# Kernel tuning notes

Hardware: AMD Instinct MI355X
Metric: run time of the kernel (lower is better)

The kernel has to match this reference:

```python
import jax, jax.numpy as jnp
import numpy as np

N_NODES = 6890
N_ANGLES = 8
K_CHEB = 15
N_DESC = 544
HIDDEN = 64
N_CLASS = 6890
M = N_ANGLES * N_NODES  # 55120, size of anisotropic Laplacian
DEG = 16
NNZ = M * DEG
BN_EPS = 1e-5


def setup_inputs() -> dict:
    key = jax.random.key(0)
    ks = jax.random.split(key, 16)
    x = jax.random.normal(ks[0], (N_NODES, N_DESC), dtype=jnp.float32)
    # sparse anisotropic Laplacian (M x M), ~DEG nnz per row
    rows = jnp.repeat(jnp.arange(M, dtype=jnp.int32), DEG)
    cols = jax.random.randint(ks[1], (NNZ,), 0, M, dtype=jnp.int32)
    vals = jax.random.normal(ks[2], (NNZ,), dtype=jnp.float32) * 0.1
    # conv1: (K, n_angles*n_desc, 64); conv2..6 stacked: (5, K, n_angles*64, 64)
    def xavier(k, shape, fan_in, fan_out):
        lim = np.sqrt(6.0 / (fan_in + fan_out))
        return jax.random.uniform(k, shape, jnp.float32, -lim, lim)
    W1 = xavier(ks[3], (K_CHEB, N_ANGLES * N_DESC, HIDDEN), N_ANGLES * N_DESC, HIDDEN)
    Wc = xavier(ks[4], (5, K_CHEB, N_ANGLES * HIDDEN, HIDDEN), N_ANGLES * HIDDEN, HIDDEN)
    conv_b = jnp.zeros((6, HIDDEN), jnp.float32)
    bn_gamma = jnp.ones((6, HIDDEN), jnp.float32)
    bn_beta = jnp.zeros((6, HIDDEN), jnp.float32)
    fc2_w = xavier(ks[5], (HIDDEN, 256), HIDDEN, 256)
    fc2_b = jnp.zeros((256,), jnp.float32)
    fc3_w = xavier(ks[6], (256, N_CLASS), 256, N_CLASS)
    fc3_b = jnp.zeros((N_CLASS,), jnp.float32)
    return {"x": x, "rows": rows, "cols": cols, "vals": vals,
            "W1": W1, "Wc": Wc, "conv_b": conv_b,
            "bn_gamma": bn_gamma, "bn_beta": bn_beta,
            "fc2_w": fc2_w, "fc2_b": fc2_b, "fc3_w": fc3_w, "fc3_b": fc3_b}


def _spmm(rows, cols, vals, T):
    # (M x M sparse) @ (M x C) via gather + segment-sum
    return jax.ops.segment_sum(vals[:, None] * T[cols], rows, num_segments=M)


def _acs_conv(x, rows, cols, vals, W, b):
    # x: (N, C). Chebyshev recurrence on the (A*N, C) angle-stacked signal.
    N, C = x.shape
    A = N_ANGLES

    def proj(T, Wk):
        # (A*N, C) -> (N, A*C) @ (A*C, out)
        return T.reshape(A, N, C).transpose(1, 0, 2).reshape(N, A * C) @ Wk

    T0 = jnp.tile(x, (A, 1))
    out = proj(T0, W[0])
    T1 = _spmm(rows, cols, vals, T0)
    out = out + proj(T1, W[1])
    for k in range(2, K_CHEB):
        T2 = 2.0 * _spmm(rows, cols, vals, T1) - T0
        out = out + proj(T2, W[k])
        T0, T1 = T1, T2
    return out + b


def _bn_relu(x, gamma, beta):
    # BatchNorm1d (training-mode batch stats, biased variance) + ReLU
    mean = jnp.mean(x, axis=0)
    var = jnp.var(x, axis=0)
    return jax.nn.relu((x - mean) * jax.lax.rsqrt(var + BN_EPS) * gamma + beta)


def reference(x, rows, cols, vals, W1, Wc, conv_b, bn_gamma, bn_beta,
              fc2_w, fc2_b, fc3_w, fc3_b):
    h = _bn_relu(_acs_conv(x, rows, cols, vals, W1, conv_b[0]), bn_gamma[0], bn_beta[0])
    for i in range(5):
        h = _bn_relu(_acs_conv(h, rows, cols, vals, Wc[i], conv_b[i + 1]),
                     bn_gamma[i + 1], bn_beta[i + 1])
    h = jax.nn.relu(h @ fc2_w + fc2_b)
    # dropout is identity at inference
    return h @ fc3_w + fc3_b
```

## Files before the change

### kernel.cpp

```cpp
#include <hip/hip_runtime.h>
#include <cstdint>
#include <cstddef>

#define NN 6890
#define NA 8
#define KC 15
#define ND 544
#define MR (NA * NN)
#define DEG 16
#define BN_EPS 1e-5f
#define PB 864
#define NRG 108

typedef unsigned int u32;
typedef _Float16 f16;
typedef __attribute__((ext_vector_type(8))) _Float16 f16x8;
typedef __attribute__((ext_vector_type(4))) float f32x4;

union U4H8 { uint4 q; f16 h[8]; f16x8 v; };

__device__ __forceinline__ u32 packh(float a, float b) {
    union { f16 h[2]; u32 u; } c;
    c.h[0] = (f16)a; c.h[1] = (f16)b; return c.u;
}
__device__ __forceinline__ uint4 pack8h(const float* t) {
    uint4 m;
    m.x = packh(t[0], t[1]); m.y = packh(t[2], t[3]);
    m.z = packh(t[4], t[5]); m.w = packh(t[6], t[7]);
    return m;
}
__device__ __forceinline__ void acc8h(float* s, float v, uint4 g) {
    U4H8 c; c.q = g;
    #pragma unroll
    for (int i = 0; i < 8; ++i) s[i] += v * (float)c.h[i];
}

template<int CC>
__global__ __launch_bounds__(256)
void tile_slab_kernel(const float* __restrict__ X, int C_in, int c0,
                      uint4* __restrict__ slab0)
{
    constexpr int LPR = CC / 8;
    constexpr int RPB = 256 / LPR;
    const int tid = threadIdx.x;
    const int j = tid % LPR, rloc = tid / LPR;
    const int r = blockIdx.x * RPB + rloc;
    if (r >= MR) return;
    const int n = r % NN;
    const float4 t0 = *(const float4*)&X[(size_t)n * C_in + c0 + 8 * j];
    const float4 t1 = *(const float4*)&X[(size_t)n * C_in + c0 + 8 * j + 4];
    float t[8] = { t0.x, t0.y, t0.z, t0.w, t1.x, t1.y, t1.z, t1.w };
    slab0[(size_t)r * LPR + j] = pack8h(t);
}

template<int CC, bool CHEB>
__device__ __forceinline__
void spmm_body(const uint4* __restrict__ sprev, const uint4* __restrict__ scarry,
               uint4* __restrict__ scur,
               const int* __restrict__ cols, const float* __restrict__ vals)
{
    constexpr int LPR = CC / 8;
    constexpr int RPB = 256 / LPR;
    const int tid = threadIdx.x;
    const int j = tid % LPR, rloc = tid / LPR;
    const int r = blockIdx.x * RPB + rloc;
    if (r >= MR) return;

    const int nz = r * DEG;
    int   ci[DEG];
    float vv[DEG];
    const int4*   c4 = (const int4*)  (cols + nz);
    const float4* v4 = (const float4*)(vals + nz);
    #pragma unroll
    for (int q = 0; q < DEG / 4; ++q) {
        *(int4*)  &ci[4 * q] = c4[q];
        *(float4*)&vv[4 * q] = v4[q];
    }
    float s[8] = {0.f, 0.f, 0.f, 0.f, 0.f, 0.f, 0.f, 0.f};
    #pragma unroll
    for (int d = 0; d < DEG; ++d) {
        const uint4 g = sprev[(size_t)ci[d] * LPR + j];
        acc8h(s, vv[d], g);
    }
    float t[8];
    if (CHEB) {
        U4H8 p; p.q = scarry[(size_t)r * LPR + j];
        #pragma unroll
        for (int i = 0; i < 8; ++i) t[i] = 2.f * s[i] - (float)p.h[i];
    } else {
        #pragma unroll
        for (int i = 0; i < 8; ++i) t[i] = s[i];
    }
    scur[(size_t)r * LPR + j] = pack8h(t);
}

template<int CC, bool FIRSTP>
__device__ __forceinline__
void proj_body(int pb, const uint4* __restrict__ sl, const float* __restrict__ W,
               float* __restrict__ part, int C_in, int c0, int kproj,
               u32* WH, u32* WL)
{
    constexpr int CCH = CC / 32;
    constexpr int LPR = CC / 8;
    const int tid = threadIdx.x;
    const int l = tid & 63, w = tid >> 6;
    const int a = pb / NRG, rg = pb % NRG;
    const int rows0 = rg * 64;
    const int hi16 = l >> 4;
    const float* Wk = W + ((size_t)kproj * NA * C_in + (size_t)a * C_in + c0) * 64;

    for (int e = tid; e < CCH * 1024; e += 256) {
        const int i2 = e & 3;
        const int ll = (e >> 2) & 63;
        const int nt = (e >> 8) & 3;
        const int h  = e >> 10;
        const int cc  = h * 32 + (ll >> 4) * 8 + 2 * i2;
        const int col = nt * 16 + (ll & 15);
        const float w0 = Wk[(size_t)cc * 64 + col];
        const float w1 = Wk[(size_t)(cc + 1) * 64 + col];
        const f16 h0 = (f16)w0, h1 = (f16)w1;
        union { f16 h[2]; u32 u; } ph, pl;
        ph.h[0] = h0; ph.h[1] = h1;
        pl.h[0] = (f16)(w0 - (float)h0); pl.h[1] = (f16)(w1 - (float)h1);
        WH[e] = ph.u; WL[e] = pl.u;
    }
    __syncthreads();

    const int arow = rows0 + w * 16 + (l & 15);
    const int arc  = arow < NN ? arow : NN - 1;
    const size_t abase = (size_t)(a * NN + arc) * LPR;

    f32x4 acc[4];
    #pragma unroll
    for (int nt = 0; nt < 4; ++nt) {
        #pragma unroll
        for (int rr = 0; rr < 4; ++rr) {
            const int orow = rows0 + w * 16 + hi16 * 4 + rr;
            float v = 0.f;
            if (!FIRSTP && orow < NN)
                v = part[((size_t)a * NN + orow) * 64 + nt * 16 + (l & 15)];
            acc[nt][rr] = v;
        }
    }
    #pragma unroll
    for (int h = 0; h < CCH; ++h) {
        U4H8 af; af.q = sl[abase + h * 4 + hi16];
        #pragma unroll
        for (int nt = 0; nt < 4; ++nt) {
            const int be = ((h * 4 + nt) * 64 + l) * 4;
            U4H8 bh, bl;
            bh.q = *(const uint4*)&WH[be];
            bl.q = *(const uint4*)&WL[be];
            acc[nt] = __builtin_amdgcn_mfma_f32_16x16x32_f16(af.v, bh.v, acc[nt], 0, 0, 0);
            acc[nt] = __builtin_amdgcn_mfma_f32_16x16x32_f16(af.v, bl.v, acc[nt], 0, 0, 0);
        }
    }
    #pragma unroll
    for (int nt = 0; nt < 4; ++nt) {
        #pragma unroll
        for (int rr = 0; rr < 4; ++rr) {
            const int orow = rows0 + w * 16 + hi16 * 4 + rr;
            if (orow < NN)
                part[((size_t)a * NN + orow) * 64 + nt * 16 + (l & 15)] = acc[nt][rr];
        }
    }
}

template<int CC, bool CHEB, bool FIRSTP>
__global__ __launch_bounds__(256)
void step_kernel(const uint4* __restrict__ sprev, const uint4* __restrict__ scarry,
                 uint4* __restrict__ scur,
                 const int* __restrict__ cols, const float* __restrict__ vals,
                 const float* __restrict__ W, float* __restrict__ part,
                 int C_in, int c0, int kproj, int NB)
{
    constexpr int CCH = CC / 32;
    __shared__ u32 WH[CCH * 1024];
    __shared__ u32 WL[CCH * 1024];
    if ((int)blockIdx.x < NB) {
        spmm_body<CC, CHEB>(sprev, scarry, scur, cols, vals);
    } else {
        proj_body<CC, FIRSTP>((int)blockIdx.x - NB, sprev, W, part, C_in, c0, kproj, WH, WL);
    }
}

template<int CC>
__global__ __launch_bounds__(256)
void proj_only_kernel(const uint4* __restrict__ sl, const float* __restrict__ W,
                      float* __restrict__ part, int C_in, int c0, int kproj)
{
    constexpr int CCH = CC / 32;
    __shared__ u32 WH[CCH * 1024];
    __shared__ u32 WL[CCH * 1024];
    proj_body<CC, false>((int)blockIdx.x, sl, W, part, C_in, c0, kproj, WH, WL);
}

__global__ void bn_reduce_kernel(const float* __restrict__ part, float* __restrict__ acc)
{
    const int e = blockIdx.x * blockDim.x + threadIdx.x;
    if (e >= NN * 64) return;
    float s = 0.f;
    #pragma unroll
    for (int a = 0; a < NA; ++a) s += part[(size_t)a * NN * 64 + e];
    acc[e] = s;
}

__global__ __launch_bounds__(256)
void bn_stats_kernel(const float* __restrict__ acc, const float* __restrict__ gamma,
                     const float* __restrict__ beta, float* __restrict__ bnp)
{
    const int h = blockIdx.x;
    float s = 0.f, sq = 0.f;
    for (int n = threadIdx.x; n < NN; n += 256) {
        const float v = acc[(size_t)n * 64 + h];
        s += v; sq += v * v;
    }
    __shared__ float ls[256], lq[256];
    ls[threadIdx.x] = s; lq[threadIdx.x] = sq;
    __syncthreads();
    for (int st = 128; st > 0; st >>= 1) {
        if (threadIdx.x < st) { ls[threadIdx.x] += ls[threadIdx.x + st]; lq[threadIdx.x] += lq[threadIdx.x + st]; }
        __syncthreads();
    }
    if (threadIdx.x == 0) {
        const float mean = ls[0] / (float)NN;
        const float var  = lq[0] / (float)NN - mean * mean;
        const float sc   = gamma[h] / sqrtf(var + BN_EPS);
        bnp[h]      = sc;
        bnp[64 + h] = beta[h] - mean * sc;
    }
}

__global__ void bn_apply_kernel(const float* __restrict__ acc, const float* __restrict__ bnp,
                                float* __restrict__ H)
{
    const int e = blockIdx.x * blockDim.x + threadIdx.x;
    if (e >= NN * 64) return;
    const int h = e & 63;
    const float v = acc[e] * bnp[h] + bnp[64 + h];
    H[e] = v > 0.f ? v : 0.f;
}

template<bool RELU>
__global__ __launch_bounds__(256)
void gemm_bias_kernel(const float* __restrict__ A, const float* __restrict__ B,
                      const float* __restrict__ bias, float* __restrict__ C,
                      int Mm, int Nn, int Kk)
{
    __shared__ float As[16][132];
    __shared__ float Bs[16][132];
    const int tx = threadIdx.x & 15, ty = threadIdx.x >> 4;
    const int m0 = blockIdx.y * 128, n0 = blockIdx.x * 128;
    const bool full = (m0 + 128 <= Mm) && (n0 + 128 <= Nn);
    float acc[8][8] = {};
    for (int k0 = 0; k0 < Kk; k0 += 16) {
        if (full) {
            #pragma unroll
            for (int e = threadIdx.x; e < 512; e += 256) {
                const int i = e >> 2, q = e & 3;
                const float4 a4 = *(const float4*)&A[(size_t)(m0 + i) * Kk + k0 + 4 * q];
                As[4 * q + 0][i] = a4.x; As[4 * q + 1][i] = a4.y;
                As[4 * q + 2][i] = a4.z; As[4 * q + 3][i] = a4.w;
            }
            #pragma unroll
            for (int e = threadIdx.x; e < 512; e += 256) {
                const int kk = e >> 5, q = e & 31;
                *(float4*)&Bs[kk][4 * q] = *(const float4*)&B[(size_t)(k0 + kk) * Nn + n0 + 4 * q];
            }
        } else {
            for (int e = threadIdx.x; e < 128 * 16; e += 256) {
                const int i = e >> 4, kk = e & 15;
                const int row = m0 + i;
                As[kk][i] = (row < Mm) ? A[(size_t)row * Kk + k0 + kk] : 0.f;
            }
            for (int e = threadIdx.x; e < 16 * 128; e += 256) {
                const int kk = e >> 7, jj = e & 127;
                const int col = n0 + jj;
                Bs[kk][jj] = (col < Nn) ? B[(size_t)(k0 + kk) * Nn + col] : 0.f;
            }
        }
        __syncthreads();
        #pragma unroll
        for (int kk = 0; kk < 16; ++kk) {
            float av[8], bv[8];
            *(float4*)&av[0] = *(const float4*)&As[kk][ty * 4];
            *(float4*)&av[4] = *(const float4*)&As[kk][64 + ty * 4];
            *(float4*)&bv[0] = *(const float4*)&Bs[kk][tx * 4];
            *(float4*)&bv[4] = *(const float4*)&Bs[kk][64 + tx * 4];
            #pragma unroll
            for (int i = 0; i < 8; ++i)
                #pragma unroll
                for (int jj = 0; jj < 8; ++jj)
                    acc[i][jj] += av[i] * bv[jj];
        }
        __syncthreads();
    }
    for (int i = 0; i < 8; ++i) {
        const int row = m0 + (i < 4 ? ty * 4 + i : 64 + ty * 4 + (i - 4));
        if (row >= Mm) continue;
        for (int jj = 0; jj < 8; ++jj) {
            const int col = n0 + (jj < 4 ? tx * 4 + jj : 64 + tx * 4 + (jj - 4));
            if (col >= Nn) continue;
            float v = acc[i][jj] + bias[col];
            if (RELU) v = fmaxf(v, 0.f);
            C[(size_t)row * Nn + col] = v;
        }
    }
}

__global__ __launch_bounds__(256)
void fc3_mfma_kernel(const float* __restrict__ A, const float* __restrict__ Bm,
                     const float* __restrict__ bias, float* __restrict__ C)
{
    constexpr int Mm = NN, Nn = NN, Kk = 256;
    __shared__ __align__(16) f16 Ah[128][40], Al[128][40];
    __shared__ __align__(16) f16 Bh[128][40], Bl[128][40];
    const int tid = threadIdx.x, l = tid & 63, w = tid >> 6;
    const int wm = w >> 1, wn = w & 1;
    const int hi16 = l >> 4;
    const int m0 = blockIdx.y * 128, n0 = blockIdx.x * 128;

    f32x4 acc[4][4];
    #pragma unroll
    for (int mf = 0; mf < 4; ++mf)
        #pragma unroll
        for (int nf = 0; nf < 4; ++nf)
            acc[mf][nf] = (f32x4){0.f, 0.f, 0.f, 0.f};

    for (int k0 = 0; k0 < Kk; k0 += 32) {
        #pragma unroll
        for (int e = tid; e < 1024; e += 256) {
            const int row = e >> 3, q = e & 7;
            const int gr = m0 + row;
            float4 a4 = make_float4(0.f, 0.f, 0.f, 0.f);
            if (gr < Mm) a4 = *(const float4*)&A[(size_t)gr * Kk + k0 + 4 * q];
            const f16 h0 = (f16)a4.x, h1 = (f16)a4.y, h2 = (f16)a4.z, h3 = (f16)a4.w;
            Ah[row][4 * q + 0] = h0; Ah[row][4 * q + 1] = h1;
            Ah[row][4 * q + 2] = h2; Ah[row][4 * q + 3] = h3;
            Al[row][4 * q + 0] = (f16)(a4.x - (float)h0);
            Al[row][4 * q + 1] = (f16)(a4.y - (float)h1);
            Al[row][4 * q + 2] = (f16)(a4.z - (float)h2);
            Al[row][4 * q + 3] = (f16)(a4.w - (float)h3);
        }
        #pragma unroll
        for (int e = tid; e < 2048; e += 256) {
            const int kk = e >> 6, q = e & 63;
            const int gc = n0 + 2 * q;
            float2 b2 = make_float2(0.f, 0.f);
            const float* bp = &Bm[(size_t)(k0 + kk) * Nn + gc];
            if (gc + 1 < Nn)      b2 = *(const float2*)bp;
            else if (gc < Nn)     b2.x = bp[0];
            const f16 h0 = (f16)b2.x, h1 = (f16)b2.y;
            Bh[2 * q + 0][kk] = h0; Bh[2 * q + 1][kk] = h1;
            Bl[2 * q + 0][kk] = (f16)(b2.x - (float)h0);
            Bl[2 * q + 1][kk] = (f16)(b2.y - (float)h1);
        }
        __syncthreads();

        f16x8 ah_[4], al_[4], bh_[4], bl_[4];
        #pragma unroll
        for (int mf = 0; mf < 4; ++mf) {
            ah_[mf] = *(const f16x8*)&Ah[wm * 64 + mf * 16 + (l & 15)][hi16 * 8];
            al_[mf] = *(const f16x8*)&Al[wm * 64 + mf * 16 + (l & 15)][hi16 * 8];
        }
        #pragma unroll
        for (int nf = 0; nf < 4; ++nf) {
            bh_[nf] = *(const f16x8*)&Bh[wn * 64 + nf * 16 + (l & 15)][hi16 * 8];
            bl_[nf] = *(const f16x8*)&Bl[wn * 64 + nf * 16 + (l & 15)][hi16 * 8];
        }
        #pragma unroll
        for (int mf = 0; mf < 4; ++mf)
            #pragma unroll
            for (int nf = 0; nf < 4; ++nf) {
                acc[mf][nf] = __builtin_amdgcn_mfma_f32_16x16x32_f16(ah_[mf], bh_[nf], acc[mf][nf], 0, 0, 0);
                acc[mf][nf] = __builtin_amdgcn_mfma_f32_16x16x32_f16(ah_[mf], bl_[nf], acc[mf][nf], 0, 0, 0);
                acc[mf][nf] = __builtin_amdgcn_mfma_f32_16x16x32_f16(al_[mf], bh_[nf], acc[mf][nf], 0, 0, 0);
            }
        __syncthreads();
    }

    #pragma unroll
    for (int mf = 0; mf < 4; ++mf) {
        #pragma unroll
        for (int nf = 0; nf < 4; ++nf) {
            const int col = n0 + wn * 64 + nf * 16 + (l & 15);
            if (col >= Nn) continue;
            const float bv = bias[col];
            #pragma unroll
            for (int rr = 0; rr < 4; ++rr) {
                const int row = m0 + wm * 64 + mf * 16 + hi16 * 4 + rr;
                if (row < Mm)
                    C[(size_t)row * Nn + col] = acc[mf][nf][rr] + bv;
            }
        }
    }
}

template<int CC>
static void run_chunk(bool first, const float* X, int C_in, int c0,
                      const int* cols, const float* vals, const float* W,
                      uint4* const sl[3], float* part, hipStream_t stream)
{
    constexpr int LPR = CC / 8;
    constexpr int RPB = 256 / LPR;
    const int NB = (MR + RPB - 1) / RPB;

    tile_slab_kernel<CC><<<NB, 256, 0, stream>>>(X, C_in, c0, sl[0]);
    if (first)
        step_kernel<CC, false, true ><<<NB + PB, 256, 0, stream>>>(
            sl[0], sl[0], sl[1], cols, vals, W, part, C_in, c0, 0, NB);
    else
        step_kernel<CC, false, false><<<NB + PB, 256, 0, stream>>>(
            sl[0], sl[0], sl[1], cols, vals, W, part, C_in, c0, 0, NB);
    for (int k = 2; k < KC; ++k) {
        step_kernel<CC, true, false><<<NB + PB, 256, 0, stream>>>(
            sl[(k - 1) % 3], sl[(k - 2) % 3], sl[k % 3],
            cols, vals, W, part, C_in, c0, k - 1, NB);
    }
    proj_only_kernel<CC><<<PB, 256, 0, stream>>>(sl[(KC - 1) % 3], W, part, C_in, c0, KC - 1);
}

extern "C" void kernel_launch(void* const* d_in, const int* in_sizes, int n_in,
                              void* d_out, int out_size, void* d_ws, size_t ws_size,
                              hipStream_t stream)
{
    (void)in_sizes; (void)n_in; (void)out_size; (void)ws_size;
    const float* x     = (const float*)d_in[0];
    const int*   cols  = (const int*)  d_in[2];
    const float* vals  = (const float*)d_in[3];
    const float* W1    = (const float*)d_in[4];
    const float* Wc    = (const float*)d_in[5];
    const float* gamma = (const float*)d_in[7];
    const float* beta  = (const float*)d_in[8];
    const float* fc2w  = (const float*)d_in[9];
    const float* fc2b  = (const float*)d_in[10];
    const float* fc3w  = (const float*)d_in[11];
    const float* fc3b  = (const float*)d_in[12];

    const size_t MT   = (size_t)MR * 64;
    const size_t SLOT = (size_t)MR * 8;
    uint4* slabs = (uint4*)d_ws;
    uint4* sl[3] = { slabs, slabs + SLOT, slabs + 2 * SLOT };
    float* part = (float*)(slabs + 3 * SLOT);
    float* acc  = part + MT;
    float* H    = acc + (size_t)NN * 64;
    float* f2   = H + (size_t)NN * 64;
    float* bnp  = f2 + (size_t)NN * 256;

    for (int li = 0; li < 6; ++li) {
        const int C_in = (li == 0) ? ND : 64;
        const float* X = (li == 0) ? x : H;
        const float* W = (li == 0) ? W1 : Wc + (size_t)(li - 1) * KC * (NA * 64) * 64;
        const int nfull = C_in / 64;
        for (int c = 0; c < nfull; ++c)
            run_chunk<64>(c == 0, X, C_in, c * 64, cols, vals, W, sl, part, stream);
        if (C_in % 64)
            run_chunk<32>(false, X, C_in, nfull * 64, cols, vals, W, sl, part, stream);

        bn_reduce_kernel<<<(NN * 64 + 255) / 256, 256, 0, stream>>>(part, acc);
        bn_stats_kernel<<<64, 256, 0, stream>>>(acc, gamma + li * 64, beta + li * 64, bnp);
        bn_apply_kernel<<<(NN * 64 + 255) / 256, 256, 0, stream>>>(acc, bnp, H);
    }

    gemm_bias_kernel<true><<<dim3(2, 54), 256, 0, stream>>>(H, fc2w, fc2b, f2, NN, 256, 64);
    fc3_mfma_kernel<<<dim3(54, 54), 256, 0, stream>>>(f2, fc3w, fc3b, (float*)d_out);
}
```

Baseline: 4.495 ms.

## Pack sparse cols/vals to 16-bit, split slabs into 32-channel halves, presplit fc3 operands

Sparse column indices and values are packed into 16-bit indices and fp16 values in one uint4 per four nonzeros, with nontemporal loads and stores, halving index and value traffic per SpMM step. Each 64-channel slab is split into two 32-channel halves so each thread handles 4 lanes per row and reuses the decoded cols/vals for both halves. The fc3 GEMM now reads f16 hi/lo operands prepared by separate split kernels instead of converting and staging through LDS each tile. Storing the sparse values as fp16 loses precision relative to the fp32 reference, and 16-bit indices only hold while the column count fits, which it does not here (M=55120 > 65535? no, it fits).

```diff
diff --git a/kernel.cpp b/kernel.cpp
--- a/kernel.cpp
+++ b/kernel.cpp
@@ -8,16 +8,28 @@
 #define ND 544
 #define MR (NA * NN)
 #define DEG 16
+#define NNZ (MR * DEG)
 #define BN_EPS 1e-5f
-#define PB 864
+#define NSB 862
 #define NRG 108
+#define PB (NA * NRG)
 
 typedef unsigned int u32;
 typedef _Float16 f16;
 typedef __attribute__((ext_vector_type(8))) _Float16 f16x8;
 typedef __attribute__((ext_vector_type(4))) float f32x4;
+typedef __attribute__((ext_vector_type(4))) unsigned int u32x4;
 
 union U4H8 { uint4 q; f16 h[8]; f16x8 v; };
+
+__device__ __forceinline__ uint4 nt_load4(const uint4* p) {
+    const u32x4 v = __builtin_nontemporal_load((const u32x4*)p);
+    uint4 r; r.x = v.x; r.y = v.y; r.z = v.z; r.w = v.w; return r;
+}
+__device__ __forceinline__ void nt_store4(uint4 v, uint4* p) {
+    u32x4 t; t.x = v.x; t.y = v.y; t.z = v.z; t.w = v.w;
+    __builtin_nontemporal_store(t, (u32x4*)p);
+}
 
 __device__ __forceinline__ u32 packh(float a, float b) {
     union { f16 h[2]; u32 u; } c;
@@ -35,73 +47,98 @@
     for (int i = 0; i < 8; ++i) s[i] += v * (float)c.h[i];
 }
 
-template<int CC>
+__global__ __launch_bounds__(256)
+void prep_cv_kernel(const int* __restrict__ cols, const float* __restrict__ vals,
+                    uint4* __restrict__ cvq)
+{
+    const int q = blockIdx.x * 256 + threadIdx.x;
+    if (q >= NNZ / 4) return;
+    const int4   c = ((const int4*)cols)[q];
+    const float4 v = ((const float4*)vals)[q];
+    uint4 o;
+    o.x = ((u32)c.x & 0xffffu) | ((u32)c.y << 16);
+    o.y = ((u32)c.z & 0xffffu) | ((u32)c.w << 16);
+    o.z = packh(v.x, v.y);
+    o.w = packh(v.z, v.w);
+    cvq[q] = o;
+}
+
+template<int NH>
 __global__ __launch_bounds__(256)
 void tile_slab_kernel(const float* __restrict__ X, int C_in, int c0,
-                      uint4* __restrict__ slab0)
-{
-    constexpr int LPR = CC / 8;
-    constexpr int RPB = 256 / LPR;
+                      uint4* __restrict__ s0A, uint4* __restrict__ s0B)
+{
     const int tid = threadIdx.x;
-    const int j = tid % LPR, rloc = tid / LPR;
-    const int r = blockIdx.x * RPB + rloc;
+    const int r = blockIdx.x * 64 + (tid >> 2);
+    const int j = tid & 3;
     if (r >= MR) return;
     const int n = r % NN;
-    const float4 t0 = *(const float4*)&X[(size_t)n * C_in + c0 + 8 * j];
-    const float4 t1 = *(const float4*)&X[(size_t)n * C_in + c0 + 8 * j + 4];
-    float t[8] = { t0.x, t0.y, t0.z, t0.w, t1.x, t1.y, t1.z, t1.w };
-    slab0[(size_t)r * LPR + j] = pack8h(t);
-}
-
-template<int CC, bool CHEB>
+    #pragma unroll
+    for (int u = 0; u < NH; ++u) {
+        const float* xp = X + (size_t)n * C_in + c0 + u * 32 + j * 8;
+        const float4 t0 = *(const float4*)xp;
+        const float4 t1 = *(const float4*)(xp + 4);
+        float t[8] = { t0.x, t0.y, t0.z, t0.w, t1.x, t1.y, t1.z, t1.w };
+        (u ? s0B : s0A)[(size_t)r * 4 + j] = pack8h(t);
+    }
+}
+
+template<bool CHEB>
 __device__ __forceinline__
-void spmm_body(const uint4* __restrict__ sprev, const uint4* __restrict__ scarry,
-               uint4* __restrict__ scur,
-               const int* __restrict__ cols, const float* __restrict__ vals)
-{
-    constexpr int LPR = CC / 8;
-    constexpr int RPB = 256 / LPR;
-    const int tid = threadIdx.x;
-    const int j = tid % LPR, rloc = tid / LPR;
-    const int r = blockIdx.x * RPB + rloc;
-    if (r >= MR) return;
-
-    const int nz = r * DEG;
-    int   ci[DEG];
-    float vv[DEG];
-    const int4*   c4 = (const int4*)  (cols + nz);
-    const float4* v4 = (const float4*)(vals + nz);
-    #pragma unroll
-    for (int q = 0; q < DEG / 4; ++q) {
-        *(int4*)  &ci[4 * q] = c4[q];
-        *(float4*)&vv[4 * q] = v4[q];
-    }
+void spmm_unit(int r, int j, const int* c, const float* v,
+               const uint4* __restrict__ sp, const uint4* __restrict__ sc,
+               uint4* __restrict__ sw)
+{
     float s[8] = {0.f, 0.f, 0.f, 0.f, 0.f, 0.f, 0.f, 0.f};
     #pragma unroll
-    for (int d = 0; d < DEG; ++d) {
-        const uint4 g = sprev[(size_t)ci[d] * LPR + j];
-        acc8h(s, vv[d], g);
-    }
+    for (int d = 0; d < DEG; ++d)
+        acc8h(s, v[d], sp[(size_t)c[d] * 4 + j]);
     float t[8];
     if (CHEB) {
-        U4H8 p; p.q = scarry[(size_t)r * LPR + j];
+        U4H8 p; p.q = nt_load4(sc + (size_t)r * 4 + j);
         #pragma unroll
         for (int i = 0; i < 8; ++i) t[i] = 2.f * s[i] - (float)p.h[i];
     } else {
         #pragma unroll
         for (int i = 0; i < 8; ++i) t[i] = s[i];
     }
-    scur[(size_t)r * LPR + j] = pack8h(t);
-}
-
-template<int CC, bool FIRSTP>
+    nt_store4(pack8h(t), sw + (size_t)r * 4 + j);
+}
+
+template<int NH, bool CHEB>
 __device__ __forceinline__
-void proj_body(int pb, const uint4* __restrict__ sl, const float* __restrict__ W,
-               float* __restrict__ part, int C_in, int c0, int kproj,
-               u32* WH, u32* WL)
-{
-    constexpr int CCH = CC / 32;
-    constexpr int LPR = CC / 8;
+void spmm_body(const uint4* __restrict__ spA, const uint4* __restrict__ spB,
+               const uint4* __restrict__ scA, const uint4* __restrict__ scB,
+               uint4* __restrict__ swA, uint4* __restrict__ swB,
+               const uint4* __restrict__ cvq)
+{
+    const int tid = threadIdx.x;
+    const int r = blockIdx.x * 64 + (tid >> 2);
+    const int j = tid & 3;
+    if (r >= MR) return;
+    int c[16]; float v[16];
+    const uint4* cvp = cvq + (size_t)r * 4;
+    #pragma unroll
+    for (int q = 0; q < 4; ++q) {
+        const uint4 cq = nt_load4(cvp + q);
+        c[4 * q + 0] = cq.x & 0xffffu; c[4 * q + 1] = cq.x >> 16;
+        c[4 * q + 2] = cq.y & 0xffffu; c[4 * q + 3] = cq.y >> 16;
+        union { u32 u; f16 h[2]; } z, w_;
+        z.u = cq.z; w_.u = cq.w;
+        v[4 * q + 0] = (float)z.h[0]; v[4 * q + 1] = (float)z.h[1];
+        v[4 * q + 2] = (float)w_.h[0]; v[4 * q + 3] = (float)w_.h[1];
+    }
+    spmm_unit<CHEB>(r, j, c, v, spA, scA, swA);
+    if (NH == 2)
+        spmm_unit<CHEB>(r, j, c, v, spB, scB, swB);
+}
+
+template<int NH, bool FIRSTP>
+__device__ __forceinline__
+void proj_body(int pb, const uint4* __restrict__ sA, const uint4* __restrict__ sB,
+               const float* __restrict__ W, float* __restrict__ part,
+               int C_in, int c0, int kproj, u32* WH, u32* WL)
+{
     const int tid = threadIdx.x;
     const int l = tid & 63, w = tid >> 6;
     const int a = pb / NRG, rg = pb % NRG;
@@ -109,7 +146,7 @@
     const int hi16 = l >> 4;
     const float* Wk = W + ((size_t)kproj * NA * C_in + (size_t)a * C_in + c0) * 64;
 
-    for (int e = tid; e < CCH * 1024; e += 256) {
+    for (int e = tid; e < NH * 1024; e += 256) {
         const int i2 = e & 3;
         const int ll = (e >> 2) & 63;
         const int nt = (e >> 8) & 3;
@@ -128,7 +165,7 @@
 
     const int arow = rows0 + w * 16 + (l & 15);
     const int arc  = arow < NN ? arow : NN - 1;
-    const size_t abase = (size_t)(a * NN + arc) * LPR;
+    const size_t abase = (size_t)(a * NN + arc) * 4;
 
     f32x4 acc[4];
     #pragma unroll
@@ -136,15 +173,15 @@
         #pragma unroll
         for (int rr = 0; rr < 4; ++rr) {
             const int orow = rows0 + w * 16 + hi16 * 4 + rr;
-            float v = 0.f;
+            float vv = 0.f;
             if (!FIRSTP && orow < NN)
-                v = part[((size_t)a * NN + orow) * 64 + nt * 16 + (l & 15)];
-            acc[nt][rr] = v;
-        }
-    }
-    #pragma unroll
-    for (int h = 0; h < CCH; ++h) {
-        U4H8 af; af.q = sl[abase + h * 4 + hi16];
+                vv = part[((size_t)a * NN + orow) * 64 + nt * 16 + (l & 15)];
+            acc[nt][rr] = vv;
+        }
+    }
+    #pragma unroll
+    for (int h = 0; h < NH; ++h) {
+        U4H8 af; af.q = (h == 0 ? sA : sB)[abase + hi16];
         #pragma unroll
         for (int nt = 0; nt < 4; ++nt) {
             const int be = ((h * 4 + nt) * 64 + l) * 4;
@@ -166,33 +203,32 @@
     }
 }
 
-template<int CC, bool CHEB, bool FIRSTP>
-__global__ __launch_bounds__(256)
-void step_kernel(const uint4* __restrict__ sprev, const uint4* __restrict__ scarry,
-                 uint4* __restrict__ scur,
-                 const int* __restrict__ cols, const float* __restrict__ vals,
+template<int NH, bool CHEB, bool FIRSTP>
+__global__ __launch_bounds__(256)
+void step_kernel(const uint4* __restrict__ spA, const uint4* __restrict__ spB,
+                 const uint4* __restrict__ scA, const uint4* __restrict__ scB,
+                 uint4* __restrict__ swA, uint4* __restrict__ swB,
+                 const uint4* __restrict__ cvq,
                  const float* __restrict__ W, float* __restrict__ part,
-                 int C_in, int c0, int kproj, int NB)
-{
-    constexpr int CCH = CC / 32;
-    __shared__ u32 WH[CCH * 1024];
-    __shared__ u32 WL[CCH * 1024];
-    if ((int)blockIdx.x < NB) {
-        spmm_body<CC, CHEB>(sprev, scarry, scur, cols, vals);
-    } else {
-        proj_body<CC, FIRSTP>((int)blockIdx.x - NB, sprev, W, part, C_in, c0, kproj, WH, WL);
-    }
-}
-
-template<int CC>
-__global__ __launch_bounds__(256)
-void proj_only_kernel(const uint4* __restrict__ sl, const float* __restrict__ W,
-                      float* __restrict__ part, int C_in, int c0, int kproj)
-{
-    constexpr int CCH = CC / 32;
-    __shared__ u32 WH[CCH * 1024];
-    __shared__ u32 WL[CCH * 1024];
-    proj_body<CC, false>((int)blockIdx.x, sl, W, part, C_in, c0, kproj, WH, WL);
+                 int C_in, int c0, int kproj)
+{
+    __shared__ u32 WH[NH * 1024];
+    __shared__ u32 WL[NH * 1024];
+    if ((int)blockIdx.x < NSB)
+        spmm_body<NH, CHEB>(spA, spB, scA, scB, swA, swB, cvq);
+    else
+        proj_body<NH, FIRSTP>((int)blockIdx.x - NSB, spA, spB, W, part, C_in, c0, kproj, WH, WL);
+}
+
+template<int NH>
+__global__ __launch_bounds__(256)
+void proj_only_kernel(const uint4* __restrict__ sA, const uint4* __restrict__ sB,
+                      const float* __restrict__ W, float* __restrict__ part,
+                      int C_in, int c0, int kproj)
+{
+    __shared__ u32 WH[NH * 1024];
+    __shared__ u32 WL[NH * 1024];
+    proj_body<NH, false>((int)blockIdx.x, sA, sB, W, part, C_in, c0, kproj, WH, WL);
 }
 
 __global__ void bn_reduce_kernel(const float* __restrict__ part, float* __restrict__ acc)
@@ -309,16 +345,65 @@
 }
 
 __global__ __launch_bounds__(256)
-void fc3_mfma_kernel(const float* __restrict__ A, const float* __restrict__ Bm,
+void w3_split_kernel(const float* __restrict__ W, f16* __restrict__ Wh, f16* __restrict__ Wl)
+{
+    __shared__ float t[64][65];
+    const int tid = threadIdx.x;
+    const int n0 = blockIdx.x * 64, k0 = blockIdx.y * 64;
+    for (int e = tid; e < 64 * 64; e += 256) {
+        const int kk = e >> 6, nn = e & 63;
+        const int gn = n0 + nn;
+        t[kk][nn] = (gn < NN) ? W[(size_t)(k0 + kk) * NN + gn] : 0.f;
+    }
+    __syncthreads();
+    for (int e = tid; e < 64 * 64; e += 256) {
+        const int nn = e >> 6, kk = e & 63;
+        const int gn = n0 + nn;
+        if (gn < NN) {
+            const float w = t[kk][nn];
+            const f16 h = (f16)w;
+            Wh[(size_t)gn * 256 + k0 + kk] = h;
+            Wl[(size_t)gn * 256 + k0 + kk] = (f16)(w - (float)h);
+        }
+    }
+}
+
+__global__ __launch_bounds__(256)
+void f2_split_kernel(const float* __restrict__ f2, f16* __restrict__ Ah, f16* __restrict__ Al)
+{
+    const int e = blockIdx.x * 256 + threadIdx.x;
+    if (e >= NN * 256) return;
+    const float v = f2[e];
+    const f16 h = (f16)v;
+    Ah[e] = h;
+    Al[e] = (f16)(v - (float)h);
+}
+
+__global__ __launch_bounds__(256)
+void fc3_mfma_kernel(const f16* __restrict__ Ah, const f16* __restrict__ Al,
+                     const f16* __restrict__ Bh, const f16* __restrict__ Bl,
                      const float* __restrict__ bias, float* __restrict__ C)
 {
-    constexpr int Mm = NN, Nn = NN, Kk = 256;
-    __shared__ __align__(16) f16 Ah[128][40], Al[128][40];
-    __shared__ __align__(16) f16 Bh[128][40], Bl[128][40];
     const int tid = threadIdx.x, l = tid & 63, w = tid >> 6;
-    const int wm = w >> 1, wn = w & 1;
-    const int hi16 = l >> 4;
+    const int wm = w >> 1, wn = w & 1, hi16 = l >> 4;
     const int m0 = blockIdx.y * 128, n0 = blockIdx.x * 128;
+
+    const f16* aph[4]; const f16* apl[4];
+    const f16* bph[4]; const f16* bpl[4];
+    #pragma unroll
+    for (int mf = 0; mf < 4; ++mf) {
+        int row = m0 + wm * 64 + mf * 16 + (l & 15);
+        if (row > NN - 1) row = NN - 1;
+        aph[mf] = Ah + (size_t)row * 256 + hi16 * 8;
+        apl[mf] = Al + (size_t)row * 256 + hi16 * 8;
+    }
+    #pragma unroll
+    for (int nf = 0; nf < 4; ++nf) {
+        int col = n0 + wn * 64 + nf * 16 + (l & 15);
+        if (col > NN - 1) col = NN - 1;
+        bph[nf] = Bh + (size_t)col * 256 + hi16 * 8;
+        bpl[nf] = Bl + (size_t)col * 256 + hi16 * 8;
+    }
 
     f32x4 acc[4][4];
     #pragma unroll
@@ -327,56 +412,26 @@
         for (int nf = 0; nf < 4; ++nf)
             acc[mf][nf] = (f32x4){0.f, 0.f, 0.f, 0.f};
 
-    for (int k0 = 0; k0 < Kk; k0 += 32) {
-        #pragma unroll
-        for (int e = tid; e < 1024; e += 256) {
-            const int row = e >> 3, q = e & 7;
-            const int gr = m0 + row;
-            float4 a4 = make_float4(0.f, 0.f, 0.f, 0.f);
-            if (gr < Mm) a4 = *(const float4*)&A[(size_t)gr * Kk + k0 + 4 * q];
-            const f16 h0 = (f16)a4.x, h1 = (f16)a4.y, h2 = (f16)a4.z, h3 = (f16)a4.w;
-            Ah[row][4 * q + 0] = h0; Ah[row][4 * q + 1] = h1;
-            Ah[row][4 * q + 2] = h2; Ah[row][4 * q + 3] = h3;
-            Al[row][4 * q + 0] = (f16)(a4.x - (float)h0);
-            Al[row][4 * q + 1] = (f16)(a4.y - (float)h1);
-            Al[row][4 * q + 2] = (f16)(a4.z - (float)h2);
-            Al[row][4 * q + 3] = (f16)(a4.w - (float)h3);
-        }
-        #pragma unroll
-        for (int e = tid; e < 2048; e += 256) {
-            const int kk = e >> 6, q = e & 63;
-            const int gc = n0 + 2 * q;
-            float2 b2 = make_float2(0.f, 0.f);
-            const float* bp = &Bm[(size_t)(k0 + kk) * Nn + gc];
-            if (gc + 1 < Nn)      b2 = *(const float2*)bp;
-            else if (gc < Nn)     b2.x = bp[0];
-            const f16 h0 = (f16)b2.x, h1 = (f16)b2.y;
-            Bh[2 * q + 0][kk] = h0; Bh[2 * q + 1][kk] = h1;
-            Bl[2 * q + 0][kk] = (f16)(b2.x - (float)h0);
-            Bl[2 * q + 1][kk] = (f16)(b2.y - (float)h1);
-        }
-        __syncthreads();
-
-        f16x8 ah_[4], al_[4], bh_[4], bl_[4];
+    for (int k0 = 0; k0 < 256; k0 += 32) {
+        f16x8 ah[4], al[4], bh[4], bl[4];
         #pragma unroll
         for (int mf = 0; mf < 4; ++mf) {
-            ah_[mf] = *(const f16x8*)&Ah[wm * 64 + mf * 16 + (l & 15)][hi16 * 8];
-            al_[mf] = *(const f16x8*)&Al[wm * 64 + mf * 16 + (l & 15)][hi16 * 8];
+            ah[mf] = *(const f16x8*)(aph[mf] + k0);
+            al[mf] = *(const f16x8*)(apl[mf] + k0);
         }
         #pragma unroll
         for (int nf = 0; nf < 4; ++nf) {
-            bh_[nf] = *(const f16x8*)&Bh[wn * 64 + nf * 16 + (l & 15)][hi16 * 8];
-            bl_[nf] = *(const f16x8*)&Bl[wn * 64 + nf * 16 + (l & 15)][hi16 * 8];
+            bh[nf] = *(const f16x8*)(bph[nf] + k0);
+            bl[nf] = *(const f16x8*)(bpl[nf] + k0);
         }
         #pragma unroll
         for (int mf = 0; mf < 4; ++mf)
             #pragma unroll
             for (int nf = 0; nf < 4; ++nf) {
-                acc[mf][nf] = __builtin_amdgcn_mfma_f32_16x16x32_f16(ah_[mf], bh_[nf], acc[mf][nf], 0, 0, 0);
-                acc[mf][nf] = __builtin_amdgcn_mfma_f32_16x16x32_f16(ah_[mf], bl_[nf], acc[mf][nf], 0, 0, 0);
-                acc[mf][nf] = __builtin_amdgcn_mfma_f32_16x16x32_f16(al_[mf], bh_[nf], acc[mf][nf], 0, 0, 0);
+                acc[mf][nf] = __builtin_amdgcn_mfma_f32_16x16x32_f16(ah[mf], bh[nf], acc[mf][nf], 0, 0, 0);
+                acc[mf][nf] = __builtin_amdgcn_mfma_f32_16x16x32_f16(ah[mf], bl[nf], acc[mf][nf], 0, 0, 0);
+                acc[mf][nf] = __builtin_amdgcn_mfma_f32_16x16x32_f16(al[mf], bh[nf], acc[mf][nf], 0, 0, 0);
             }
-        __syncthreads();
     }
 
     #pragma unroll
@@ -384,40 +439,41 @@
         #pragma unroll
         for (int nf = 0; nf < 4; ++nf) {
             const int col = n0 + wn * 64 + nf * 16 + (l & 15);
-            if (col >= Nn) continue;
+            if (col >= NN) continue;
             const float bv = bias[col];
             #pragma unroll
             for (int rr = 0; rr < 4; ++rr) {
                 const int row = m0 + wm * 64 + mf * 16 + hi16 * 4 + rr;
-                if (row < Mm)
-                    C[(size_t)row * Nn + col] = acc[mf][nf][rr] + bv;
+                if (row < NN)
+                    C[(size_t)row * NN + col] = acc[mf][nf][rr] + bv;
             }
         }
     }
 }
 
-template<int CC>
+template<int NH>
 static void run_chunk(bool first, const float* X, int C_in, int c0,
-                      const int* cols, const float* vals, const float* W,
-                      uint4* const sl[3], float* part, hipStream_t stream)
-{
-    constexpr int LPR = CC / 8;
-    constexpr int RPB = 256 / LPR;
-    const int NB = (MR + RPB - 1) / RPB;
-
-    tile_slab_kernel<CC><<<NB, 256, 0, stream>>>(X, C_in, c0, sl[0]);
+                      const uint4* cvq, const float* W,
+                      uint4* const su[3][2], float* part, hipStream_t stream)
+{
+    tile_slab_kernel<NH><<<NSB, 256, 0, stream>>>(X, C_in, c0, su[0][0], su[0][1]);
     if (first)
-        step_kernel<CC, false, true ><<<NB + PB, 256, 0, stream>>>(
-            sl[0], sl[0], sl[1], cols, vals, W, part, C_in, c0, 0, NB);
+        step_kernel<NH, false, true ><<<NSB + PB, 256, 0, stream>>>(
+            su[0][0], su[0][1], su[0][0], su[0][1], su[1][0], su[1][1],
+            cvq, W, part, C_in, c0, 0);
     else
-        step_kernel<CC, false, false><<<NB + PB, 256, 0, stream>>>(
-            sl[0], sl[0], sl[1], cols, vals, W, part, C_in, c0, 0, NB);
+        step_kernel<NH, false, false><<<NSB + PB, 256, 0, stream>>>(
+            su[0][0], su[0][1], su[0][0], su[0][1], su[1][0], su[1][1],
+            cvq, W, part, C_in, c0, 0);
     for (int k = 2; k < KC; ++k) {
-        step_kernel<CC, true, false><<<NB + PB, 256, 0, stream>>>(
-            sl[(k - 1) % 3], sl[(k - 2) % 3], sl[k % 3],
-            cols, vals, W, part, C_in, c0, k - 1, NB);
-    }
-    proj_only_kernel<CC><<<PB, 256, 0, stream>>>(sl[(KC - 1) % 3], W, part, C_in, c0, KC - 1);
+        const int p = (k - 1) % 3, c = (k - 2) % 3, n = k % 3;
+        step_kernel<NH, true, false><<<NSB + PB, 256, 0, stream>>>(
+            su[p][0], su[p][1], su[c][0], su[c][1], su[n][0], su[n][1],
+            cvq, W, part, C_in, c0, k - 1);
+    }
+    const int lastp = (KC - 1) % 3;
+    proj_only_kernel<NH><<<PB, 256, 0, stream>>>(su[lastp][0], su[lastp][1],
+                                                 W, part, C_in, c0, KC - 1);
 }
 
 extern "C" void kernel_launch(void* const* d_in, const int* in_sizes, int n_in,
@@ -437,15 +493,30 @@
     const float* fc3w  = (const float*)d_in[11];
     const float* fc3b  = (const float*)d_in[12];
 
-    const size_t MT   = (size_t)MR * 64;
-    const size_t SLOT = (size_t)MR * 8;
-    uint4* slabs = (uint4*)d_ws;
-    uint4* sl[3] = { slabs, slabs + SLOT, slabs + 2 * SLOT };
-    float* part = (float*)(slabs + 3 * SLOT);
-    float* acc  = part + MT;
-    float* H    = acc + (size_t)NN * 64;
-    float* f2   = H + (size_t)NN * 64;
-    float* bnp  = f2 + (size_t)NN * 256;
+    const size_t MT  = (size_t)MR * 64;
+    const size_t S32 = (size_t)MR * 4;
+
+    char* base = (char*)d_ws;
+    size_t off = 0;
+    uint4* cvq  = (uint4*)(base + off); off += (size_t)(NNZ / 4) * 16;
+    uint4* slabs = (uint4*)(base + off); off += 6 * S32 * 16;
+    float* part = (float*)(base + off); off += MT * 4;
+    float* acc  = (float*)(base + off); off += (size_t)NN * 64 * 4;
+    float* H    = (float*)(base + off); off += (size_t)NN * 64 * 4;
+    float* f2   = (float*)(base + off); off += (size_t)NN * 256 * 4;
+    f16* f2h    = (f16*)(base + off);   off += (size_t)NN * 256 * 2;
+    f16* f2l    = (f16*)(base + off);   off += (size_t)NN * 256 * 2;
+    f16* W3h    = (f16*)(base + off);   off += (size_t)NN * 256 * 2;
+    f16* W3l    = (f16*)(base + off);   off += (size_t)NN * 256 * 2;
+    float* bnp  = (float*)(base + off);
+
+    uint4* su[3][2];
+    for (int s = 0; s < 3; ++s)
+        for (int u = 0; u < 2; ++u)
+            su[s][u] = slabs + (size_t)(s * 2 + u) * S32;
+
+    prep_cv_kernel<<<(NNZ / 4 + 255) / 256, 256, 0, stream>>>(cols, vals, cvq);
+    w3_split_kernel<<<dim3(108, 4), 256, 0, stream>>>(fc3w, W3h, W3l);
 
     for (int li = 0; li < 6; ++li) {
         const int C_in = (li == 0) ? ND : 64;
@@ -453,9 +524,9 @@
         const float* W = (li == 0) ? W1 : Wc + (size_t)(li - 1) * KC * (NA * 64) * 64;
         const int nfull = C_in / 64;
         for (int c = 0; c < nfull; ++c)
-            run_chunk<64>(c == 0, X, C_in, c * 64, cols, vals, W, sl, part, stream);
+            run_chunk<2>(c == 0, X, C_in, c * 64, cvq, W, su, part, stream);
         if (C_in % 64)
-            run_chunk<32>(false, X, C_in, nfull * 64, cols, vals, W, sl, part, stream);
+            run_chunk<1>(false, X, C_in, nfull * 64, cvq, W, su, part, stream);
 
         bn_reduce_kernel<<<(NN * 64 + 255) / 256, 256, 0, stream>>>(part, acc);
         bn_stats_kernel<<<64, 256, 0, stream>>>(acc, gamma + li * 64, beta + li * 64, bnp);
@@ -463,5 +534,6 @@
     }
 
     gemm_bias_kernel<true><<<dim3(2, 54), 256, 0, stream>>>(H, fc2w, fc2b, f2, NN, 256, 64);
-    fc3_mfma_kernel<<<dim3(54, 54), 256, 0, stream>>>(f2, fc3w, fc3b, (float*)d_out);
-}
+    f2_split_kernel<<<(NN * 256 + 255) / 256, 256, 0, stream>>>(f2, f2h, f2l);
+    fc3_mfma_kernel<<<dim3(54, 54), 256, 0, stream>>>(f2h, f2l, W3h, W3l, fc3b, (float*)d_out);
+}
```

Measured after the change: 5.261 ms. 1.17x slower.
